# Kernel optimization log

Hardware: AMD Instinct MI355X
Metric: run time of the kernel (lower is better)

Reference implementation:

```python
import jax, jax.numpy as jnp
import numpy as np

N_NODES = 50000
N_EDGES = 600000
N_GRAPHS = 1000
IN_DIM = 16
HID = 128
DESC = 17
NUM_LAYERS = 3
BN_EPS = 1e-5


def setup_inputs() -> dict:
    key = jax.random.key(0)
    ks = jax.random.split(key, 16)
    x = jax.random.normal(ks[0], (N_NODES, IN_DIM), dtype=jnp.float32)
    edge_index = jax.random.randint(ks[1], (2, N_EDGES), 0, N_NODES, dtype=jnp.int32)
    edge_attr = jax.random.normal(ks[2], (N_EDGES, HID), dtype=jnp.float32)
    batch = jnp.sort(jax.random.randint(ks[3], (N_NODES,), 0, N_GRAPHS, dtype=jnp.int32))
    mol_desc = jax.random.normal(ks[4], (N_GRAPHS, DESC), dtype=jnp.float32)
    s = 1.0 / np.sqrt(HID)
    Wp = jax.random.normal(ks[5], (IN_DIM, HID), dtype=jnp.float32) / np.sqrt(IN_DIM)
    bp = jnp.zeros((HID,), jnp.float32)
    W1 = jax.random.normal(ks[6], (NUM_LAYERS, HID, HID), dtype=jnp.float32) * s
    b1 = jnp.zeros((NUM_LAYERS, HID), jnp.float32)
    W2 = jax.random.normal(ks[7], (NUM_LAYERS, HID, HID), dtype=jnp.float32) * s
    b2 = jnp.zeros((NUM_LAYERS, HID), jnp.float32)
    gamma = jnp.ones((NUM_LAYERS, HID), jnp.float32)
    beta = jnp.zeros((NUM_LAYERS, HID), jnp.float32)
    Wf = jax.random.normal(ks[8], (HID + DESC, 1), dtype=jnp.float32) / np.sqrt(HID + DESC)
    bf = jnp.zeros((1,), jnp.float32)
    return dict(x=x, edge_index=edge_index, edge_attr=edge_attr, batch=batch,
                mol_desc=mol_desc, Wp=Wp, bp=bp, W1=W1, b1=b1, W2=W2, b2=b2,
                gamma=gamma, beta=beta, Wf=Wf, bf=bf)


def reference(x, edge_index, edge_attr, batch, mol_desc,
              Wp, bp, W1, b1, W2, b2, gamma, beta, Wf, bf):
    src, dst = edge_index[0], edge_index[1]
    h = x @ Wp + bp  # [N, HID]
    for l in range(NUM_LAYERS):
        # GINEConv: aggr_i = sum_j relu(h_j + e_ij); out = MLP((1+eps)*h + aggr), eps=0
        msg = jax.nn.relu(h[src] + edge_attr)                       # [E, HID] gather
        aggr = jax.ops.segment_sum(msg, dst, num_segments=N_NODES)  # scatter-add
        z = h + aggr
        z = jax.nn.relu(z @ W1[l] + b1[l]) @ W2[l] + b2[l]
        # BatchNorm1d (training-mode batch statistics)
        mean = jnp.mean(z, axis=0)
        var = jnp.var(z, axis=0)
        z = (z - mean) * jax.lax.rsqrt(var + BN_EPS) * gamma[l] + beta[l]
        h = jax.nn.relu(z)  # dropout = identity (eval)
    # global mean pool per graph
    sums = jax.ops.segment_sum(h, batch, num_segments=N_GRAPHS)
    counts = jax.ops.segment_sum(jnp.ones((N_NODES,), h.dtype), batch, num_segments=N_GRAPHS)
    pooled = sums / jnp.maximum(counts, 1.0)[:, None]
    feats = jnp.concatenate([pooled, mol_desc], axis=1)  # [G, HID+DESC]
    return (feats @ Wf + bf).squeeze(-1)  # [G]
```

## Files before the change

### kernel.cpp

```cpp
#include <hip/hip_runtime.h>
#include <hip/hip_bf16.h>

#define NN 50000
#define NE 600000
#define NG 1000
#define IND 16
#define HID 128
#define DESCD 17
#define NL 3
#define BN_EPS 1e-5f
#define NB_SCAN 196

typedef short s16x8 __attribute__((ext_vector_type(8)));
typedef float f32x4 __attribute__((ext_vector_type(4)));
typedef int   i32x4 __attribute__((ext_vector_type(4)));
typedef __hip_bfloat16 bfp16;
typedef __hip_bfloat162 bfp162;

__device__ __forceinline__ float b2f(short s) {
    return __uint_as_float(((unsigned int)(unsigned short)s) << 16);
}

__global__ __launch_bounds__(256) void k_hist(const int* __restrict__ dst,
                                              int* __restrict__ deg) {
    int e = blockIdx.x * blockDim.x + threadIdx.x;
    if (e >= NE) return;
    atomicAdd(&deg[dst[e]], 1);
}

__global__ __launch_bounds__(256) void k_part(const int* __restrict__ deg,
                                              int* __restrict__ partials) {
    __shared__ int sh[256];
    int i = blockIdx.x * 256 + threadIdx.x;
    sh[threadIdx.x] = (i < NN) ? deg[i] : 0;
    __syncthreads();
    for (int o = 128; o > 0; o >>= 1) {
        if (threadIdx.x < o) sh[threadIdx.x] += sh[threadIdx.x + o];
        __syncthreads();
    }
    if (threadIdx.x == 0) partials[blockIdx.x] = sh[0];
}

__global__ __launch_bounds__(256) void k_scanpart(const int* __restrict__ partials,
                                                  int* __restrict__ poffs) {
    __shared__ int sh[256];
    int t = threadIdx.x;
    int v = (t < NB_SCAN) ? partials[t] : 0;
    sh[t] = v;
    __syncthreads();
    for (int o = 1; o < 256; o <<= 1) {
        int tmp = (t >= o) ? sh[t - o] : 0;
        __syncthreads();
        sh[t] += tmp;
        __syncthreads();
    }
    if (t < NB_SCAN) poffs[t] = sh[t] - v;
}

__global__ __launch_bounds__(256) void k_scatter(const int* __restrict__ deg,
                                                 const int* __restrict__ poffs,
                                                 int* __restrict__ rowptr,
                                                 int* __restrict__ cursor) {
    __shared__ int sh[256];
    int b = blockIdx.x, t = threadIdx.x;
    int i = b * 256 + t;
    int v = (i < NN) ? deg[i] : 0;
    sh[t] = v;
    __syncthreads();
    for (int o = 1; o < 256; o <<= 1) {
        int tmp = (t >= o) ? sh[t - o] : 0;
        __syncthreads();
        sh[t] += tmp;
        __syncthreads();
    }
    int excl = sh[t] - v + poffs[b];
    if (i < NN) {
        rowptr[i] = excl;
        cursor[i] = excl;
        if (i == NN - 1) rowptr[NN] = excl + v;
    }
}

__global__ __launch_bounds__(256) void k_fill(const int* __restrict__ src,
                                              const int* __restrict__ dst,
                                              int* __restrict__ cursor,
                                              int2* __restrict__ perm) {
    int e = blockIdx.x * blockDim.x + threadIdx.x;
    if (e >= NE) return;
    int pos = atomicAdd(&cursor[dst[e]], 1);
    perm[pos] = make_int2(e, src[e]);
}

__global__ __launch_bounds__(256) void k_projwprep(const float* __restrict__ x,
                                                   const float* __restrict__ Wp,
                                                   const float* __restrict__ bp,
                                                   bfp16* __restrict__ h,
                                                   const float* __restrict__ W1,
                                                   const float* __restrict__ W2,
                                                   bfp16* __restrict__ Wt,
                                                   int projBlocks) {
    if (blockIdx.x < (unsigned)projBlocks) {
        int idx = blockIdx.x * blockDim.x + threadIdx.x;
        if (idx >= NN * HID) return;
        int row = idx >> 7, col = idx & 127;
        const float* xr = x + (size_t)row * IND;
        float acc = bp[col];
#pragma unroll
        for (int k = 0; k < IND; k++) acc += xr[k] * Wp[k * HID + col];
        h[idx] = __float2bfloat16(acc);
    } else {
        int id = (blockIdx.x - projBlocks) * blockDim.x + threadIdx.x;
        if (id >= 6 * HID * HID) return;
        int m = id >> 14;
        int rem = id & 16383;
        int n = rem >> 7, k = rem & 127;
        const float* Wsrc = (m < 3) ? (W1 + (size_t)m * HID * HID)
                                    : (W2 + (size_t)(m - 3) * HID * HID);
        Wt[id] = __float2bfloat16(Wsrc[k * HID + n]);
    }
}

template <int MODE, bool BN>
__global__ __launch_bounds__(256) void k_aggr(const bfp16* __restrict__ hz,
                                              const float* __restrict__ ea,
                                              bfp16* __restrict__ eab,
                                              const int2* __restrict__ perm,
                                              const int* __restrict__ rowptr,
                                              const float* __restrict__ stats,
                                              const float* __restrict__ gamma,
                                              const float* __restrict__ beta,
                                              bfp16* __restrict__ z) {
    int nid = (blockIdx.x * blockDim.x + threadIdx.x) >> 6;
    int lane = threadIdx.x & 63;
    if (nid >= NN) return;
    const int slot = lane >> 4;
    const int c0 = (lane & 15) << 3;

    float sc[8], sf[8];
    if (BN) {
        const float invn = 1.f / NN;
#pragma unroll
        for (int j = 0; j < 8; j++) {
            int c = c0 + j;
            float m = stats[c] * invn;
            float v = stats[128 + c] * invn - m * m;
            sc[j] = rsqrtf(v + BN_EPS) * gamma[c];
            sf[j] = beta[c] - m * sc[j];
        }
    }

    float acc[8];
#pragma unroll
    for (int j = 0; j < 8; j++) acc[j] = 0.f;

    auto body = [&](int i) {
        int2 pr = perm[i];
        float a[8];
        if (MODE == 1) {
            f32x4 a0 = __builtin_nontemporal_load(
                (const f32x4*)&ea[(size_t)pr.x * HID + c0]);
            f32x4 a1 = __builtin_nontemporal_load(
                (const f32x4*)&ea[(size_t)pr.x * HID + c0 + 4]);
            a[0] = a0.x; a[1] = a0.y; a[2] = a0.z; a[3] = a0.w;
            a[4] = a1.x; a[5] = a1.y; a[6] = a1.z; a[7] = a1.w;
            bfp162 p0 = __float22bfloat162_rn(make_float2(a[0], a[1]));
            bfp162 p1 = __float22bfloat162_rn(make_float2(a[2], a[3]));
            bfp162 p2 = __float22bfloat162_rn(make_float2(a[4], a[5]));
            bfp162 p3 = __float22bfloat162_rn(make_float2(a[6], a[7]));
            i32x4 o;
            o.x = *reinterpret_cast<int*>(&p0);
            o.y = *reinterpret_cast<int*>(&p1);
            o.z = *reinterpret_cast<int*>(&p2);
            o.w = *reinterpret_cast<int*>(&p3);
            *(i32x4*)&eab[(size_t)i * HID + c0] = o;
        } else {
            s16x8 av = *(const s16x8*)&eab[(size_t)i * HID + c0];
#pragma unroll
            for (int j = 0; j < 8; j++) a[j] = b2f(av[j]);
        }
        s16x8 hv = *(const s16x8*)&hz[(size_t)pr.y * HID + c0];
#pragma unroll
        for (int j = 0; j < 8; j++) {
            float hf = b2f(hv[j]);
            if (BN) hf = fmaxf(hf * sc[j] + sf[j], 0.f);
            acc[j] += fmaxf(a[j] + hf, 0.f);
        }
    };

    int beg = rowptr[nid], end = rowptr[nid + 1];
    int i = beg + slot;
    for (; i + 4 < end; i += 8) {
        body(i);
        body(i + 4);
    }
    if (i < end) body(i);

#pragma unroll
    for (int j = 0; j < 8; j++) {
        acc[j] += __shfl_xor(acc[j], 16);
        acc[j] += __shfl_xor(acc[j], 32);
    }

    if (lane < 16) {
        s16x8 hv = *(const s16x8*)&hz[(size_t)nid * HID + c0];
        bfp162 pk[4];
#pragma unroll
        for (int j = 0; j < 4; j++) {
            float h0 = b2f(hv[2 * j]);
            float h1 = b2f(hv[2 * j + 1]);
            if (BN) {
                h0 = fmaxf(h0 * sc[2 * j] + sf[2 * j], 0.f);
                h1 = fmaxf(h1 * sc[2 * j + 1] + sf[2 * j + 1], 0.f);
            }
            pk[j] = __float22bfloat162_rn(make_float2(acc[2 * j] + h0,
                                                      acc[2 * j + 1] + h1));
        }
        i32x4 o;
        o.x = *reinterpret_cast<int*>(&pk[0]);
        o.y = *reinterpret_cast<int*>(&pk[1]);
        o.z = *reinterpret_cast<int*>(&pk[2]);
        o.w = *reinterpret_cast<int*>(&pk[3]);
        *(i32x4*)&z[(size_t)nid * HID + c0] = o;
    }
}

__global__ __launch_bounds__(256) void k_mlp(const bfp16* __restrict__ A,
                                             const bfp16* __restrict__ Wt1,
                                             const bfp16* __restrict__ Wt2,
                                             const float* __restrict__ b1,
                                             const float* __restrict__ b2,
                                             bfp16* __restrict__ z2,
                                             float* __restrict__ stats,
                                             int N) {
    __shared__ __align__(16) short sW1[128 * 128];
    __shared__ __align__(16) short sW2[128 * 128];
    __shared__ __align__(16) short sA[64 * 128];
    const int t = threadIdx.x;
    const int rowBase = blockIdx.x * 64;

    const short* W1g = (const short*)Wt1;
    const short* W2g = (const short*)Wt2;
    for (int g = t; g < 2048; g += 256) {
        int nrow = g >> 4, s = g & 15;
        int sw = nrow * 128 + ((s ^ (nrow & 7)) << 3);
        *(float4*)&sW1[sw] = *(const float4*)&W1g[g * 8];
        *(float4*)&sW2[sw] = *(const float4*)&W2g[g * 8];
    }
    const short* Ag = (const short*)A;
    for (int g = t; g < 1024; g += 256) {
        int r = g >> 4, s = g & 15;
        float4 v = make_float4(0.f, 0.f, 0.f, 0.f);
        if (rowBase + r < N) v = *(const float4*)&Ag[(size_t)(rowBase + r) * 128 + s * 8];
        *(float4*)&sA[r * 128 + ((s ^ (r & 7)) << 3)] = v;
    }
    __syncthreads();

    const int w = t >> 6, lane = t & 63;
    const int l15 = lane & 15, lhi = lane >> 4;
    const int arow = (w << 4) + l15;
    const int abase = arow * 128, asw = arow & 7;
    const int bsw = l15 & 7;

    f32x4 acc[8];
#pragma unroll
    for (int c = 0; c < 8; c++) acc[c] = (f32x4){0.f, 0.f, 0.f, 0.f};
#pragma unroll
    for (int kk = 0; kk < 4; kk++) {
        int kslot = kk * 4 + lhi;
        s16x8 af = *(const s16x8*)&sA[abase + ((kslot ^ asw) << 3)];
#pragma unroll
        for (int c = 0; c < 8; c++) {
            s16x8 bfr = *(const s16x8*)&sW1[(c * 16 + l15) * 128 + ((kslot ^ bsw) << 3)];
            acc[c] = __builtin_amdgcn_mfma_f32_16x16x32_bf16(af, bfr, acc[c], 0, 0, 0);
        }
    }
    __syncthreads();

    {
        const int rowb = (w << 4);
#pragma unroll
        for (int c = 0; c < 8; c++) {
            float bb = b1[c * 16 + l15];
            int col = c * 16 + l15;
#pragma unroll
            for (int r = 0; r < 4; r++) {
                int row = rowb + lhi * 4 + r;
                float v = fmaxf(acc[c][r] + bb, 0.f);
                bfp16 bv = __float2bfloat16(v);
                sA[row * 128 + ((((col >> 3)) ^ (row & 7)) << 3) + (col & 7)] =
                    *reinterpret_cast<short*>(&bv);
            }
        }
    }
    __syncthreads();

    f32x4 acc2[8];
#pragma unroll
    for (int c = 0; c < 8; c++) acc2[c] = (f32x4){0.f, 0.f, 0.f, 0.f};
#pragma unroll
    for (int kk = 0; kk < 4; kk++) {
        int kslot = kk * 4 + lhi;
        s16x8 af = *(const s16x8*)&sA[abase + ((kslot ^ asw) << 3)];
#pragma unroll
        for (int c = 0; c < 8; c++) {
            s16x8 bfr = *(const s16x8*)&sW2[(c * 16 + l15) * 128 + ((kslot ^ bsw) << 3)];
            acc2[c] = __builtin_amdgcn_mfma_f32_16x16x32_bf16(af, bfr, acc2[c], 0, 0, 0);
        }
    }

    const int rb = rowBase + (w << 4) + lhi * 4;
    float scol[8], qcol[8];
#pragma unroll
    for (int c = 0; c < 8; c++) {
        float bb = b2[c * 16 + l15];
        float s = 0.f, q = 0.f;
#pragma unroll
        for (int r = 0; r < 4; r++) {
            int row = rb + r;
            float v = acc2[c][r] + bb;
            if (row < N) {
                z2[(size_t)row * 128 + c * 16 + l15] = __float2bfloat16(v);
                s += v;
                q += v * v;
            }
        }
        scol[c] = s;
        qcol[c] = q;
    }
#pragma unroll
    for (int c = 0; c < 8; c++) {
        scol[c] += __shfl_xor(scol[c], 16);
        scol[c] += __shfl_xor(scol[c], 32);
        qcol[c] += __shfl_xor(qcol[c], 16);
        qcol[c] += __shfl_xor(qcol[c], 32);
    }
    __syncthreads();
    float* sStat = (float*)sA;
    if (lane < 16) {
#pragma unroll
        for (int c = 0; c < 8; c++) {
            sStat[w * 256 + c * 16 + lane] = scol[c];
            sStat[w * 256 + 128 + c * 16 + lane] = qcol[c];
        }
    }
    __syncthreads();
    if (t < 128) {
        float ss = sStat[t] + sStat[256 + t] + sStat[512 + t] + sStat[768 + t];
        float qq = sStat[128 + t] + sStat[384 + t] + sStat[640 + t] + sStat[896 + t];
        atomicAdd(&stats[t], ss);
        atomicAdd(&stats[128 + t], qq);
    }
}

__global__ __launch_bounds__(256) void k_finalpool(const bfp16* __restrict__ z2,
                                                   const float* __restrict__ stats,
                                                   const float* __restrict__ gamma,
                                                   const float* __restrict__ beta,
                                                   const int* __restrict__ batch,
                                                   const float* __restrict__ mol,
                                                   const float* __restrict__ Wf,
                                                   const float* __restrict__ bfp,
                                                   float* __restrict__ out) {
    int gid = (blockIdx.x * blockDim.x + threadIdx.x) >> 6;
    int lane = threadIdx.x & 63;
    if (gid >= NG) return;
    const int f = lane * 2;

    const float invn = 1.f / NN;
    float m0 = stats[f] * invn;
    float v0 = stats[128 + f] * invn - m0 * m0;
    float sc0 = rsqrtf(v0 + BN_EPS) * gamma[f];
    float sf0 = beta[f] - m0 * sc0;
    float m1 = stats[f + 1] * invn;
    float v1 = stats[128 + f + 1] * invn - m1 * m1;
    float sc1 = rsqrtf(v1 + BN_EPS) * gamma[f + 1];
    float sf1 = beta[f + 1] - m1 * sc1;

    int lo = 0, hi = NN;
    while (lo < hi) { int m = (lo + hi) >> 1; if (batch[m] < gid) lo = m + 1; else hi = m; }
    int lb = lo;
    hi = NN;
    while (lo < hi) { int m = (lo + hi) >> 1; if (batch[m] <= gid) lo = m + 1; else hi = m; }
    int cnt = lo - lb;

    float sx = 0.f, sy = 0.f;
    for (int n = lb; n < lo; n++) {
        float2 v = __bfloat1622float2(*(const bfp162*)&z2[(size_t)n * HID + f]);
        sx += fmaxf(v.x * sc0 + sf0, 0.f);
        sy += fmaxf(v.y * sc1 + sf1, 0.f);
    }
    float inv = 1.f / fmaxf((float)cnt, 1.f);
    float acc = sx * inv * Wf[f] + sy * inv * Wf[f + 1];
    if (lane < DESCD) acc += mol[(size_t)gid * DESCD + lane] * Wf[HID + lane];
#pragma unroll
    for (int o = 32; o > 0; o >>= 1) acc += __shfl_down(acc, o);
    if (lane == 0) out[gid] = acc + bfp[0];
}

extern "C" void kernel_launch(void* const* d_in, const int* in_sizes, int n_in,
                              void* d_out, int out_size, void* d_ws, size_t ws_size,
                              hipStream_t stream) {
    const float* x     = (const float*)d_in[0];
    const int*   ei    = (const int*)d_in[1];
    const float* ea    = (const float*)d_in[2];
    const int*   batch = (const int*)d_in[3];
    const float* mol   = (const float*)d_in[4];
    const float* Wp    = (const float*)d_in[5];
    const float* bp    = (const float*)d_in[6];
    const float* W1    = (const float*)d_in[7];
    const float* b1    = (const float*)d_in[8];
    const float* W2    = (const float*)d_in[9];
    const float* b2    = (const float*)d_in[10];
    const float* gamma = (const float*)d_in[11];
    const float* beta  = (const float*)d_in[12];
    const float* Wf    = (const float*)d_in[13];
    const float* bf_   = (const float*)d_in[14];
    float* out = (float*)d_out;

    char* p = (char*)d_ws;
    size_t off = 0;
    auto alloc = [&](size_t bytes) {
        char* q = p + off;
        off = (off + bytes + 255) & ~(size_t)255;
        return q;
    };
    bfp16* h      = (bfp16*)alloc((size_t)NN * HID * 2);
    bfp16* z      = (bfp16*)alloc((size_t)NN * HID * 2);
    bfp16* z2     = (bfp16*)alloc((size_t)NN * HID * 2);
    bfp16* Wt     = (bfp16*)alloc((size_t)6 * HID * HID * 2);
    int2*  perm   = (int2*)alloc((size_t)NE * 8);
    int*   rowptr = (int*)alloc((NN + 16) * 4);
    int*   cursor = (int*)alloc(NN * 4);
    int*   partials = (int*)alloc(NB_SCAN * 4);
    int*   poffs    = (int*)alloc(NB_SCAN * 4);
    size_t zoff = off;
    int*   deg    = (int*)alloc(NN * 4);
    float* stats3 = (float*)alloc(3 * 256 * 4);
    size_t zlen = off - zoff;
    bfp16* eab    = (bfp16*)alloc((size_t)NE * HID * 2);

    const int* src = ei;
    const int* dst = ei + NE;

    (void)hipMemsetAsync(p + zoff, 0, zlen, stream);
    k_hist<<<(NE + 255) / 256, 256, 0, stream>>>(dst, deg);
    k_part<<<NB_SCAN, 256, 0, stream>>>(deg, partials);
    k_scanpart<<<1, 256, 0, stream>>>(partials, poffs);
    k_scatter<<<NB_SCAN, 256, 0, stream>>>(deg, poffs, rowptr, cursor);
    k_fill<<<(NE + 255) / 256, 256, 0, stream>>>(src, dst, cursor, perm);
    {
        const int projBlocks = (NN * HID) / 256;
        const int wprepBlocks = (6 * HID * HID + 255) / 256;
        k_projwprep<<<projBlocks + wprepBlocks, 256, 0, stream>>>(
            x, Wp, bp, h, W1, W2, Wt, projBlocks);
    }

    const int aggrGrid = (NN * 64) / 256;
    const int mlpGrid = (NN + 63) / 64;
    for (int l = 0; l < NL; l++) {
        if (l == 0)
            k_aggr<1, false><<<aggrGrid, 256, 0, stream>>>(
                h, ea, eab, perm, rowptr, nullptr, nullptr, nullptr, z);
        else
            k_aggr<2, true><<<aggrGrid, 256, 0, stream>>>(
                z2, nullptr, eab, perm, rowptr, stats3 + (l - 1) * 256,
                gamma + (l - 1) * HID, beta + (l - 1) * HID, z);
        k_mlp<<<mlpGrid, 256, 0, stream>>>(
            z, Wt + (size_t)l * HID * HID, Wt + (size_t)(3 + l) * HID * HID,
            b1 + l * HID, b2 + l * HID, z2, stats3 + l * 256, NN);
    }

    k_finalpool<<<(NG * 64) / 256, 256, 0, stream>>>(
        z2, stats3 + 2 * 256, gamma + 2 * HID, beta + 2 * HID,
        batch, mol, Wf, bf_, out);
}
```

Before: 431.6 us.

## Merge fill with projection kernel and reuse one LDS weight buffer in MLP

The CSR fill step now runs inside the projection and weight-prep launch as extra blocks, which removes one kernel launch and lets the independent work overlap. The MLP kernel keeps a single 32KB shared weight buffer and loads W2 into it after the first GEMM, instead of holding W1 and W2 together. This cuts LDS per block from 80KB to 48KB so more blocks can be resident per CU. The cost is that the W2 load is no longer overlapped with the W1 load and now sits after the first GEMM.

```diff
diff --git a/kernel.cpp b/kernel.cpp
--- a/kernel.cpp
+++ b/kernel.cpp
@@ -81,26 +81,25 @@
     }
 }
 
-__global__ __launch_bounds__(256) void k_fill(const int* __restrict__ src,
-                                              const int* __restrict__ dst,
-                                              int* __restrict__ cursor,
-                                              int2* __restrict__ perm) {
-    int e = blockIdx.x * blockDim.x + threadIdx.x;
-    if (e >= NE) return;
-    int pos = atomicAdd(&cursor[dst[e]], 1);
-    perm[pos] = make_int2(e, src[e]);
-}
-
-__global__ __launch_bounds__(256) void k_projwprep(const float* __restrict__ x,
-                                                   const float* __restrict__ Wp,
-                                                   const float* __restrict__ bp,
-                                                   bfp16* __restrict__ h,
-                                                   const float* __restrict__ W1,
-                                                   const float* __restrict__ W2,
-                                                   bfp16* __restrict__ Wt,
-                                                   int projBlocks) {
-    if (blockIdx.x < (unsigned)projBlocks) {
-        int idx = blockIdx.x * blockDim.x + threadIdx.x;
+__global__ __launch_bounds__(256) void k_fillproj(const int* __restrict__ src,
+                                                  const int* __restrict__ dst,
+                                                  int* __restrict__ cursor,
+                                                  int2* __restrict__ perm,
+                                                  const float* __restrict__ x,
+                                                  const float* __restrict__ Wp,
+                                                  const float* __restrict__ bp,
+                                                  bfp16* __restrict__ h,
+                                                  const float* __restrict__ W1,
+                                                  const float* __restrict__ W2,
+                                                  bfp16* __restrict__ Wt,
+                                                  int fillBlocks, int projBlocks) {
+    if (blockIdx.x < (unsigned)fillBlocks) {
+        int e = blockIdx.x * blockDim.x + threadIdx.x;
+        if (e >= NE) return;
+        int pos = atomicAdd(&cursor[dst[e]], 1);
+        perm[pos] = make_int2(e, src[e]);
+    } else if (blockIdx.x < (unsigned)(fillBlocks + projBlocks)) {
+        int idx = (blockIdx.x - fillBlocks) * blockDim.x + threadIdx.x;
         if (idx >= NN * HID) return;
         int row = idx >> 7, col = idx & 127;
         const float* xr = x + (size_t)row * IND;
@@ -109,7 +108,7 @@
         for (int k = 0; k < IND; k++) acc += xr[k] * Wp[k * HID + col];
         h[idx] = __float2bfloat16(acc);
     } else {
-        int id = (blockIdx.x - projBlocks) * blockDim.x + threadIdx.x;
+        int id = (blockIdx.x - fillBlocks - projBlocks) * blockDim.x + threadIdx.x;
         if (id >= 6 * HID * HID) return;
         int m = id >> 14;
         int rem = id & 16383;
@@ -232,8 +231,7 @@
                                              bfp16* __restrict__ z2,
                                              float* __restrict__ stats,
                                              int N) {
-    __shared__ __align__(16) short sW1[128 * 128];
-    __shared__ __align__(16) short sW2[128 * 128];
+    __shared__ __align__(16) short sW[128 * 128];
     __shared__ __align__(16) short sA[64 * 128];
     const int t = threadIdx.x;
     const int rowBase = blockIdx.x * 64;
@@ -243,8 +241,7 @@
     for (int g = t; g < 2048; g += 256) {
         int nrow = g >> 4, s = g & 15;
         int sw = nrow * 128 + ((s ^ (nrow & 7)) << 3);
-        *(float4*)&sW1[sw] = *(const float4*)&W1g[g * 8];
-        *(float4*)&sW2[sw] = *(const float4*)&W2g[g * 8];
+        *(float4*)&sW[sw] = *(const float4*)&W1g[g * 8];
     }
     const short* Ag = (const short*)A;
     for (int g = t; g < 1024; g += 256) {
@@ -270,7 +267,7 @@
         s16x8 af = *(const s16x8*)&sA[abase + ((kslot ^ asw) << 3)];
 #pragma unroll
         for (int c = 0; c < 8; c++) {
-            s16x8 bfr = *(const s16x8*)&sW1[(c * 16 + l15) * 128 + ((kslot ^ bsw) << 3)];
+            s16x8 bfr = *(const s16x8*)&sW[(c * 16 + l15) * 128 + ((kslot ^ bsw) << 3)];
             acc[c] = __builtin_amdgcn_mfma_f32_16x16x32_bf16(af, bfr, acc[c], 0, 0, 0);
         }
     }
@@ -292,6 +289,11 @@
             }
         }
     }
+    for (int g = t; g < 2048; g += 256) {
+        int nrow = g >> 4, s = g & 15;
+        int sw = nrow * 128 + ((s ^ (nrow & 7)) << 3);
+        *(float4*)&sW[sw] = *(const float4*)&W2g[g * 8];
+    }
     __syncthreads();
 
     f32x4 acc2[8];
@@ -303,7 +305,7 @@
         s16x8 af = *(const s16x8*)&sA[abase + ((kslot ^ asw) << 3)];
 #pragma unroll
         for (int c = 0; c < 8; c++) {
-            s16x8 bfr = *(const s16x8*)&sW2[(c * 16 + l15) * 128 + ((kslot ^ bsw) << 3)];
+            s16x8 bfr = *(const s16x8*)&sW[(c * 16 + l15) * 128 + ((kslot ^ bsw) << 3)];
             acc2[c] = __builtin_amdgcn_mfma_f32_16x16x32_bf16(af, bfr, acc2[c], 0, 0, 0);
         }
     }
@@ -447,12 +449,13 @@
     k_part<<<NB_SCAN, 256, 0, stream>>>(deg, partials);
     k_scanpart<<<1, 256, 0, stream>>>(partials, poffs);
     k_scatter<<<NB_SCAN, 256, 0, stream>>>(deg, poffs, rowptr, cursor);
-    k_fill<<<(NE + 255) / 256, 256, 0, stream>>>(src, dst, cursor, perm);
     {
+        const int fillBlocks = (NE + 255) / 256;
         const int projBlocks = (NN * HID) / 256;
         const int wprepBlocks = (6 * HID * HID + 255) / 256;
-        k_projwprep<<<projBlocks + wprepBlocks, 256, 0, stream>>>(
-            x, Wp, bp, h, W1, W2, Wt, projBlocks);
+        k_fillproj<<<fillBlocks + projBlocks + wprepBlocks, 256, 0, stream>>>(
+            src, dst, cursor, perm, x, Wp, bp, h, W1, W2, Wt,
+            fillBlocks, projBlocks);
     }
 
     const int aggrGrid = (NN * 64) / 256;
```

Measured after the change: 442.1 us. 1.02x slower.
